# Kernel tuning notes

Hardware: AMD Instinct MI355X
Metric: run time of the kernel (lower is better)

The kernel has to match this reference:

```python
import jax, jax.numpy as jnp
import numpy as np

EPS = 1e-5   # torch nn.LayerNorm default
H = 12       # num_heads


def layernorm(x, w, b):
    m = jnp.mean(x, axis=-1, keepdims=True)
    v = jnp.var(x, axis=-1, keepdims=True)
    return (x - m) * jax.lax.rsqrt(v + EPS) * w + b


def mha(x, qkv_w, proj_w, proj_b):
    # MemEffAttention math (qkv_bias=False, proj_bias=True), block-diagonal mask
    # over equal-length sequences == independent per-row attention.
    B, N, D = x.shape
    hd = D // H
    qkv = jnp.einsum('bnd,ed->bne', x, qkv_w).reshape(B, N, 3, H, hd)
    q, k, v = qkv[:, :, 0], qkv[:, :, 1], qkv[:, :, 2]
    scale = hd ** -0.5
    attn = jnp.einsum('bnhd,bmhd->bhnm', q * scale, k)     # [B,H,N,N]
    attn = jax.nn.softmax(attn, axis=-1)
    o = jnp.einsum('bhnm,bmhd->bnhd', attn, v).reshape(B, N, D)
    return jnp.einsum('bnd,ed->bne', o, proj_w) + proj_b


def block(x, ln1_w, ln1_b, qkv_w, proj_w, proj_b, ln2_w, ln2_b, fc1_w, fc1_b, fc2_w, fc2_b):
    # x = x + attn(norm1(x)); x = x + mlp(norm2(x))  (ls1/ls2 = Identity, eval mode)
    x = x + mha(layernorm(x, ln1_w, ln1_b), qkv_w, proj_w, proj_b)
    h = layernorm(x, ln2_w, ln2_b)
    h = jax.nn.gelu(jnp.einsum('bnd,ed->bne', h, fc1_w) + fc1_b, approximate=False)
    h = jnp.einsum('bne,de->bnd', h, fc2_w) + fc2_b
    return x + h


def setup_inputs() -> dict:
    key = jax.random.key(0)
    ks = jax.random.split(key, 8)
    D, Dff = 768, 3072
    s = lambda k, shape, sc: jax.random.normal(k, shape, jnp.float32) * sc
    return {
        'x1': s(ks[0], (8, 1370, D), 1.0),
        'x2': s(ks[1], (8, 257, D), 1.0),
        'ln1_w': jnp.ones((D,), jnp.float32), 'ln1_b': jnp.zeros((D,), jnp.float32),
        'qkv_w': s(ks[2], (3 * D, D), 0.02),
        'proj_w': s(ks[3], (D, D), 0.02), 'proj_b': jnp.zeros((D,), jnp.float32),
        'ln2_w': jnp.ones((D,), jnp.float32), 'ln2_b': jnp.zeros((D,), jnp.float32),
        'fc1_w': s(ks[4], (Dff, D), 0.02), 'fc1_b': jnp.zeros((Dff,), jnp.float32),
        'fc2_w': s(ks[5], (D, Dff), 0.02), 'fc2_b': jnp.zeros((D,), jnp.float32),
    }


def reference(x1, x2, ln1_w, ln1_b, qkv_w, proj_w, proj_b, ln2_w, ln2_b,
              fc1_w, fc1_b, fc2_w, fc2_b):
    # forward_nested (eval path): block-diagonal attention over nested groups,
    # which factorizes into per-group batched attention; return the
    # concatenated token stream (same values as attn_bias.split output).
    params = (ln1_w, ln1_b, qkv_w, proj_w, proj_b, ln2_w, ln2_b,
              fc1_w, fc1_b, fc2_w, fc2_b)
    o1 = block(x1, *params)
    o2 = block(x2, *params)
    D = x1.shape[-1]
    return jnp.concatenate([o1.reshape(-1, D), o2.reshape(-1, D)], axis=0)
```

## Files before the change

kernel.cpp:

```cpp
#include <hip/hip_runtime.h>
#include <hip/hip_bf16.h>

typedef __attribute__((ext_vector_type(8))) short bf16x8;
typedef __attribute__((ext_vector_type(4))) float f32x4;
typedef __attribute__((ext_vector_type(16))) float f32x16;

#define GL_LDS16(g, l)                                                        \
  __builtin_amdgcn_global_load_lds((const __attribute__((address_space(1))) void*)(g), \
                                   (__attribute__((address_space(3))) void*)(l), 16, 0, 0)

__device__ __forceinline__ ushort f2bf(float f) {
  union { float f; unsigned u; } x; x.f = f;
  unsigned r = x.u + 0x7fffu + ((x.u >> 16) & 1u);
  return (ushort)(r >> 16);
}

__device__ __forceinline__ int xcd_remap(int bid, int nwg) {
  int q = nwg >> 3, r = nwg & 7;
  int xcd = bid & 7, idx = bid >> 3;
  return (xcd < r ? xcd * (q + 1) : r * (q + 1) + (xcd - r) * q) + idx;
}

__global__ void cvt4_kernel(const float* __restrict__ i0, const float* __restrict__ i1,
                            const float* __restrict__ i2, const float* __restrict__ i3,
                            int n0, int n1, int n2, int n3,
                            ushort* __restrict__ out) {
  int c1 = n0 >> 2, c2 = (n0 + n1) >> 2, c3 = (n0 + n1 + n2) >> 2,
      nt = (n0 + n1 + n2 + n3) >> 2;
  int i = blockIdx.x * blockDim.x + threadIdx.x;
  int stride = gridDim.x * blockDim.x;
  for (; i < nt; i += stride) {
    float4 v;
    if (i < c1) v = ((const float4*)i0)[i];
    else if (i < c2) v = ((const float4*)i1)[i - c1];
    else if (i < c3) v = ((const float4*)i2)[i - c2];
    else v = ((const float4*)i3)[i - c3];
    ushort4 o;
    o.x = f2bf(v.x); o.y = f2bf(v.y); o.z = f2bf(v.z); o.w = f2bf(v.w);
    ((ushort4*)out)[i] = o;
  }
}

__global__ __launch_bounds__(256) void ln_kernel(
    const float* __restrict__ x1, const float* __restrict__ x2, int M1, int MT,
    const float* __restrict__ w, const float* __restrict__ b,
    ushort* __restrict__ out) {
  int row = blockIdx.x * 4 + (threadIdx.x >> 6);
  if (row >= MT) return;
  int lane = threadIdx.x & 63;
  const float* xr = (row < M1) ? x1 + (size_t)row * 768
                               : x2 + (size_t)(row - M1) * 768;
  float4 v[3];
  float s = 0.f, sq = 0.f;
#pragma unroll
  for (int i = 0; i < 3; i++) {
    v[i] = *(const float4*)(xr + i * 256 + lane * 4);
    s += v[i].x + v[i].y + v[i].z + v[i].w;
    sq += v[i].x * v[i].x + v[i].y * v[i].y + v[i].z * v[i].z + v[i].w * v[i].w;
  }
#pragma unroll
  for (int m = 1; m < 64; m <<= 1) { s += __shfl_xor(s, m); sq += __shfl_xor(sq, m); }
  float mean = s * (1.f / 768.f);
  float var = sq * (1.f / 768.f) - mean * mean;
  float rstd = rsqrtf(var + 1e-5f);
  ushort* orow = out + (size_t)row * 768;
#pragma unroll
  for (int i = 0; i < 3; i++) {
    int d = i * 256 + lane * 4;
    float4 wv = *(const float4*)(w + d);
    float4 bv = *(const float4*)(b + d);
    ushort4 o;
    o.x = f2bf((v[i].x - mean) * rstd * wv.x + bv.x);
    o.y = f2bf((v[i].y - mean) * rstd * wv.y + bv.y);
    o.z = f2bf((v[i].z - mean) * rstd * wv.z + bv.z);
    o.w = f2bf((v[i].w - mean) * rstd * wv.w + bv.w);
    *(ushort4*)(orow + d) = o;
  }
}

template <int MODE, int K, int NCOL>
__global__ __launch_bounds__(256) void gemm_tile(
    const ushort* __restrict__ A, const ushort* __restrict__ W,
    const float* __restrict__ bias, void* __restrict__ outp,
    int M, int N) {
  __shared__ ushort lA[128 * 64];
  __shared__ ushort lB[128 * 64];
  const int t = threadIdx.x;
  const int lane = t & 63, wave = t >> 6;
  const int l15 = lane & 15, lg = lane >> 4;
  const int waveM = wave >> 1, waveN = wave & 1;
  const int g = xcd_remap(blockIdx.x, gridDim.x);
  const int rowBlk = (g / NCOL) * 128;
  const int colBlk = (g % NCOL) * 128;
  const int srow = t >> 3;
  const int schunk = t & 7;

  f32x4 acc[4][4] = {};

#pragma unroll 1
  for (int k0 = 0; k0 < K; k0 += 64) {
    if (k0) __syncthreads();
#pragma unroll
    for (int i = 0; i < 4; i++) {
      int row = i * 32 + srow;
      int gch = schunk ^ (row & 7);
      GL_LDS16(A + (size_t)(rowBlk + row) * K + k0 + gch * 8,
               &lA[row * 64 + schunk * 8]);
      GL_LDS16(W + (size_t)(colBlk + row) * K + k0 + gch * 8,
               &lB[row * 64 + schunk * 8]);
    }
    __syncthreads();
#pragma unroll
    for (int kk = 0; kk < 2; kk++) {
      bf16x8 af[4], bfr[4];
#pragma unroll
      for (int m = 0; m < 4; m++) {
        int row = waveM * 64 + m * 16 + l15;
        af[m] = *(const bf16x8*)&lA[row * 64 + ((kk * 32 + lg * 8) ^ ((row & 7) << 3))];
      }
#pragma unroll
      for (int c = 0; c < 4; c++) {
        int row = waveN * 64 + c * 16 + l15;
        bfr[c] = *(const bf16x8*)&lB[row * 64 + ((kk * 32 + lg * 8) ^ ((row & 7) << 3))];
      }
      __builtin_amdgcn_s_setprio(1);
#pragma unroll
      for (int m = 0; m < 4; m++)
#pragma unroll
        for (int c = 0; c < 4; c++)
          acc[m][c] = __builtin_amdgcn_mfma_f32_16x16x32_bf16(af[m], bfr[c], acc[m][c], 0, 0, 0);
      __builtin_amdgcn_s_setprio(0);
    }
  }

  const float qsc = (MODE == 0 && colBlk < 768) ? 0.18033688011112042f : 1.f;
#pragma unroll
  for (int m = 0; m < 4; m++) {
    int rowB = rowBlk + waveM * 64 + m * 16 + lg * 4;
#pragma unroll
    for (int c = 0; c < 4; c++) {
      int col = colBlk + waveN * 64 + c * 16 + l15;
      float bv = (MODE == 2) ? bias[col] : 0.f;
#pragma unroll
      for (int j = 0; j < 4; j++) {
        int r = rowB + j;
        if (r < M) {
          float v = acc[m][c][j] + bv;
          size_t idx = (size_t)r * N + col;
          if (MODE == 2) {
            float gl = 0.5f * v * (1.f + erff(v * 0.70710678118f));
            ((ushort*)outp)[idx] = f2bf(gl);
          } else {
            ((ushort*)outp)[idx] = f2bf(v * qsc);
          }
        }
      }
    }
  }
}

template <int K, int NCOL>
__global__ __launch_bounds__(256) void gemm_tile64(
    const ushort* __restrict__ A, const ushort* __restrict__ W,
    const float* __restrict__ bias, const float* __restrict__ res1,
    const float* __restrict__ res2, int resSplit,
    float* __restrict__ outp, int M, int N) {
  __shared__ ushort lA[64 * 64];
  __shared__ ushort lB[128 * 64];
  const int t = threadIdx.x;
  const int lane = t & 63, wave = t >> 6;
  const int l15 = lane & 15, lg = lane >> 4;
  const int waveM = wave >> 1, waveN = wave & 1;
  const int g = xcd_remap(blockIdx.x, gridDim.x);
  const int rowBlk = (g / NCOL) * 64;
  const int colBlk = (g % NCOL) * 128;
  const int srow = t >> 3;
  const int schunk = t & 7;

  f32x4 acc[2][4] = {};

#pragma unroll 1
  for (int k0 = 0; k0 < K; k0 += 64) {
    if (k0) __syncthreads();
#pragma unroll
    for (int i = 0; i < 2; i++) {
      int row = i * 32 + srow;
      int gch = schunk ^ (row & 7);
      GL_LDS16(A + (size_t)(rowBlk + row) * K + k0 + gch * 8,
               &lA[row * 64 + schunk * 8]);
    }
#pragma unroll
    for (int i = 0; i < 4; i++) {
      int row = i * 32 + srow;
      int gch = schunk ^ (row & 7);
      GL_LDS16(W + (size_t)(colBlk + row) * K + k0 + gch * 8,
               &lB[row * 64 + schunk * 8]);
    }
    __syncthreads();
#pragma unroll
    for (int kk = 0; kk < 2; kk++) {
      bf16x8 af[2], bfr[4];
#pragma unroll
      for (int m = 0; m < 2; m++) {
        int row = waveM * 32 + m * 16 + l15;
        af[m] = *(const bf16x8*)&lA[row * 64 + ((kk * 32 + lg * 8) ^ ((row & 7) << 3))];
      }
#pragma unroll
      for (int c = 0; c < 4; c++) {
        int row = waveN * 64 + c * 16 + l15;
        bfr[c] = *(const bf16x8*)&lB[row * 64 + ((kk * 32 + lg * 8) ^ ((row & 7) << 3))];
      }
      __builtin_amdgcn_s_setprio(1);
#pragma unroll
      for (int m = 0; m < 2; m++)
#pragma unroll
        for (int c = 0; c < 4; c++)
          acc[m][c] = __builtin_amdgcn_mfma_f32_16x16x32_bf16(af[m], bfr[c], acc[m][c], 0, 0, 0);
      __builtin_amdgcn_s_setprio(0);
    }
  }

#pragma unroll
  for (int m = 0; m < 2; m++) {
    int rowB = rowBlk + waveM * 32 + m * 16 + lg * 4;
#pragma unroll
    for (int c = 0; c < 4; c++) {
      int col = colBlk + waveN * 64 + c * 16 + l15;
      float bv = bias[col];
#pragma unroll
      for (int j = 0; j < 4; j++) {
        int r = rowB + j;
        if (r < M) {
          size_t idx = (size_t)r * N + col;
          float rv = (r < resSplit) ? res1[idx]
                                    : res2[(size_t)(r - resSplit) * N + col];
          outp[idx] = acc[m][c][j] + bv + rv;
        }
      }
    }
  }
}

__global__ __launch_bounds__(256) void prep_kernel(
    const ushort* __restrict__ qkv, ushort* __restrict__ kt2,
    ushort* __restrict__ vt2, int N1, int N2, int nkv1, int nkv2, int M1) {
  __shared__ ushort lT[64 * 68];
  const int t = threadIdx.x;
  const int bhg = blockIdx.x;
  const int kv = blockIdx.y;
  const int part = bhg >= 96;
  const int bh = part ? bhg - 96 : bhg;
  const int N = part ? N2 : N1;
  const int nkv = part ? nkv2 : nkv1;
  if (kv >= nkv) return;
  const size_t rowbase = part ? (size_t)M1 : 0;
  const int b = bh / 12, h = bh % 12;
  const int k0 = kv * 64;
  const ushort* Kp = qkv + (rowbase + (size_t)b * N) * 2304 + 768 + h * 64;
  const ushort* Vp = Kp + 768;
  size_t tbase = (part ? (size_t)96 * nkv1 : 0) + (size_t)bh * nkv + kv;
  ushort* ktile = kt2 + tbase * 4096;
  ushort* vtile = vt2 + tbase * 4096;
#pragma unroll
  for (int p = 0; p < 2; p++) {
    int s = p * 256 + t;
    int chunk = s >> 6, krow = s & 63;
    ushort4 v0 = {0, 0, 0, 0}, v1 = {0, 0, 0, 0};
    if (k0 + krow < N) {
      const ushort* src = Kp + (size_t)(k0 + krow) * 2304 + chunk * 8;
      v0 = *(const ushort4*)src;
      v1 = *(const ushort4*)(src + 4);
    }
    *(ushort4*)&ktile[s * 8] = v0;
    *(ushort4*)&ktile[s * 8 + 4] = v1;
  }
#pragma unroll
  for (int p = 0; p < 2; p++) {
    int nl = p * 32 + (t >> 3);
    int dc = t & 7;
    ushort4 v0 = {0, 0, 0, 0}, v1 = {0, 0, 0, 0};
    if (k0 + nl < N) {
      const ushort* src = Vp + (size_t)(k0 + nl) * 2304 + dc * 8;
      v0 = *(const ushort4*)src;
      v1 = *(const ushort4*)(src + 4);
    }
    *(ushort4*)&lT[nl * 68 + dc * 8] = v0;
    *(ushort4*)&lT[nl * 68 + dc * 8 + 4] = v1;
  }
  __syncthreads();
#pragma unroll
  for (int p = 0; p < 2; p++) {
    int s = p * 256 + t;
    int kchunk = s >> 6, d = s & 63;
    ushort o[8];
#pragma unroll
    for (int j = 0; j < 8; j++) o[j] = lT[(kchunk * 8 + j) * 68 + d];
    *(ushort4*)&vtile[s * 8] = *(ushort4*)o;
    *(ushort4*)&vtile[s * 8 + 4] = *(ushort4*)(o + 4);
  }
}

#define ATTN_STAGE(buf, kvi)                                                   \
  do {                                                                         \
    _Pragma("unroll") for (int p = 0; p < 2; p++) {                            \
      int s = p * 256 + t;                                                     \
      GL_LDS16(tK + (size_t)(kvi) * 4096 + s * 8, &lK[buf][s * 8]);            \
      GL_LDS16(tV + (size_t)(kvi) * 4096 + s * 8, &lV[buf][s * 8]);            \
    }                                                                          \
  } while (0)

__global__ __launch_bounds__(256) void attn_kernel(
    const ushort* __restrict__ qkv, const ushort* __restrict__ kt2,
    const ushort* __restrict__ vt2, ushort* __restrict__ o_out,
    int N1, int N2, int nkv1, int nkv2, int M1) {
  __shared__ ushort lK[2][4096];
  __shared__ ushort lV[2][4096];
  const int t = threadIdx.x;
  const int lane = t & 63, wave = t >> 6;
  const int l31 = lane & 31, hi = lane >> 5;
  const int bhg = blockIdx.x;
  const int part = bhg >= 96;
  const int bh = part ? bhg - 96 : bhg;
  const int N = part ? N2 : N1;
  const int nkv = part ? nkv2 : nkv1;
  const int qb = blockIdx.y * 128;
  if (qb >= N) return;
  const size_t rowbase = part ? (size_t)M1 : 0;
  const int b = bh / 12, h = bh % 12;
  const ushort* Qp = qkv + (rowbase + (size_t)b * N) * 2304 + h * 64;
  const size_t tboff = (part ? (size_t)96 * nkv1 : 0) + (size_t)bh * nkv;
  const ushort* tK = kt2 + tboff * 4096;
  const ushort* tV = vt2 + tboff * 4096;

  const int qrow = min(qb + wave * 32 + l31, N - 1);
  bf16x8 qf[4];
#pragma unroll
  for (int kc = 0; kc < 4; kc++)
    qf[kc] = *(const bf16x8*)(Qp + (size_t)qrow * 2304 + kc * 16 + hi * 8);

  union { unsigned u[4]; bf16x8 v; } ones;
#pragma unroll
  for (int i = 0; i < 4; i++) ones.u[i] = 0x3F803F80u;

  f32x16 oacc[2] = {};
  f32x16 osum = {};

  ATTN_STAGE(0, 0);
  __syncthreads();
  for (int kv = 0; kv < nkv; kv++) {
    int cur = kv & 1;
    if (kv + 1 < nkv) ATTN_STAGE(cur ^ 1, kv + 1);
    const bool fullTile = (kv * 64 + 64 <= N);
    f32x16 sacc0 = {}, sacc1 = {};
    __builtin_amdgcn_s_setprio(1);
#pragma unroll
    for (int kc = 0; kc < 4; kc++) {
      bf16x8 kf0 = *(const bf16x8*)&lK[cur][(((kc * 2 + hi) << 6) + l31) * 8];
      bf16x8 kf1 = *(const bf16x8*)&lK[cur][(((kc * 2 + hi) << 6) + 32 + l31) * 8];
      sacc0 = __builtin_amdgcn_mfma_f32_32x32x16_bf16(kf0, qf[kc], sacc0, 0, 0, 0);
      sacc1 = __builtin_amdgcn_mfma_f32_32x32x16_bf16(kf1, qf[kc], sacc1, 0, 0, 0);
    }
    __builtin_amdgcn_s_setprio(0);
    float z[32];
#pragma unroll
    for (int r = 0; r < 16; r++) { z[r] = sacc0[r]; z[16 + r] = sacc1[r]; }
    if (!fullTile) {
#pragma unroll
      for (int i = 0; i < 32; i++) {
        int kg = kv * 64 + (i >> 4) * 32 + (i & 3) + (((i & 15) >> 2) << 3) + (hi << 2);
        if (kg >= N) z[i] = -1e30f;
      }
    }
#pragma unroll
    for (int i = 0; i < 32; i++) z[i] = exp2f(z[i]);
#pragma unroll
    for (int kt = 0; kt < 2; kt++) {
      unsigned w0[4], w1[4];
#pragma unroll
      for (int rr = 0; rr < 4; rr++) {
        asm("v_cvt_pk_bf16_f32 %0, %1, %2" : "=v"(w0[rr]) : "v"(z[kt * 16 + 4 * rr]), "v"(z[kt * 16 + 4 * rr + 1]));
        asm("v_cvt_pk_bf16_f32 %0, %1, %2" : "=v"(w1[rr]) : "v"(z[kt * 16 + 4 * rr + 2]), "v"(z[kt * 16 + 4 * rr + 3]));
      }
#pragma unroll
      for (int kc2 = 0; kc2 < 2; kc2++) {
        unsigned ua = w0[2 * kc2], ub = w0[2 * kc2 + 1];
        unsigned uc = w1[2 * kc2], ud = w1[2 * kc2 + 1];
        asm("v_permlane32_swap_b32 %0, %1" : "+&v"(ua), "+v"(ub));
        asm("v_permlane32_swap_b32 %0, %1" : "+&v"(uc), "+v"(ud));
        union { unsigned u[4]; bf16x8 v; } pa;
        pa.u[0] = ua; pa.u[1] = uc; pa.u[2] = ub; pa.u[3] = ud;
        int kcg = kt * 2 + kc2;
        __builtin_amdgcn_s_setprio(1);
#pragma unroll
        for (int dt = 0; dt < 2; dt++) {
          bf16x8 vf = *(const bf16x8*)&lV[cur][(((kcg * 2 + hi) << 6) + dt * 32 + l31) * 8];
          oacc[dt] = __builtin_amdgcn_mfma_f32_32x32x16_bf16(pa.v, vf, oacc[dt], 0, 0, 0);
        }
        osum = __builtin_amdgcn_mfma_f32_32x32x16_bf16(pa.v, ones.v, osum, 0, 0, 0);
        __builtin_amdgcn_s_setprio(0);
      }
    }
    __syncthreads();
  }
#pragma unroll
  for (int r = 0; r < 16; r++) {
    int q = qb + wave * 32 + (r & 3) + ((r >> 2) << 3) + (hi << 2);
    if (q < N) {
      float inv;
      asm("v_rcp_f32 %0, %1" : "=v"(inv) : "v"(osum[r]));
      ushort* orow = o_out + (rowbase + (size_t)b * N + q) * 768 + h * 64;
      orow[l31] = f2bf(oacc[0][r] * inv);
      orow[32 + l31] = f2bf(oacc[1][r] * inv);
    }
  }
}

extern "C" void kernel_launch(void* const* d_in, const int* in_sizes, int n_in,
                              void* d_out, int out_size, void* d_ws, size_t ws_size,
                              hipStream_t stream) {
  const float* x1 = (const float*)d_in[0];
  const float* x2 = (const float*)d_in[1];
  const float* ln1_w = (const float*)d_in[2];
  const float* ln1_b = (const float*)d_in[3];
  const float* qkv_w = (const float*)d_in[4];
  const float* proj_w = (const float*)d_in[5];
  const float* proj_b = (const float*)d_in[6];
  const float* ln2_w = (const float*)d_in[7];
  const float* ln2_b = (const float*)d_in[8];
  const float* fc1_w = (const float*)d_in[9];
  const float* fc1_b = (const float*)d_in[10];
  const float* fc2_w = (const float*)d_in[11];
  const float* fc2_b = (const float*)d_in[12];
  float* out = (float*)d_out;

  const int N1 = 1370, N2 = 257;
  const int M1 = 8 * N1, M2 = 8 * N2;
  const int MT = M1 + M2;
  const int MPAD = 13056;
  const int nkv1 = 22, nkv2 = 5;

  char* ws = (char*)d_ws;
  ushort* wq = (ushort*)ws;   ws += (size_t)2304 * 768 * 2;
  ushort* wp = (ushort*)ws;   ws += (size_t)768 * 768 * 2;
  ushort* w1 = (ushort*)ws;   ws += (size_t)3072 * 768 * 2;
  ushort* w2 = (ushort*)ws;   ws += (size_t)768 * 3072 * 2;
  ushort* bufA = (ushort*)ws;   ws += (size_t)MPAD * 768 * 2;
  ushort* bufQKV = (ushort*)ws; ws += (size_t)MPAD * 2304 * 2;
  ushort* bufFF = (ushort*)ws;  ws += (size_t)MPAD * 3072 * 2;
  const size_t nTiles = (size_t)96 * (nkv1 + nkv2);
  ushort* kt2 = bufFF;
  ushort* vt2 = bufFF + nTiles * 4096;

  cvt4_kernel<<<2048, 256, 0, stream>>>(qkv_w, proj_w, fc1_w, fc2_w,
                                        2304 * 768, 768 * 768, 3072 * 768, 768 * 3072, wq);

  ln_kernel<<<(MT + 3) / 4, 256, 0, stream>>>(x1, x2, M1, MT, ln1_w, ln1_b, bufA);
  gemm_tile<0, 768, 18><<<(MPAD / 128) * 18, 256, 0, stream>>>(
      bufA, wq, nullptr, bufQKV, MT, 2304);
  prep_kernel<<<dim3(192, nkv1), 256, 0, stream>>>(bufQKV, kt2, vt2, N1, N2, nkv1, nkv2, M1);
  attn_kernel<<<dim3(192, 11), 256, 0, stream>>>(
      bufQKV, kt2, vt2, bufA, N1, N2, nkv1, nkv2, M1);
  gemm_tile64<768, 6><<<(MPAD / 64) * 6, 256, 0, stream>>>(
      bufA, wp, proj_b, x1, x2, M1, out, MT, 768);
  ln_kernel<<<(MT + 3) / 4, 256, 0, stream>>>(out, out, MT, MT, ln2_w, ln2_b, bufA);
  gemm_tile<2, 768, 24><<<(MPAD / 128) * 24, 256, 0, stream>>>(
      bufA, w1, fc1_b, bufFF, MT, 3072);
  gemm_tile64<3072, 6><<<(MPAD / 64) * 6, 256, 0, stream>>>(
      bufFF, w2, fc2_b, out, nullptr, MT, out, MT, 768);
}
```

Baseline: 459.0 us.

## Double-buffer LDS in GEMM kernels with vmcnt-based prefetch pipelining

Both GEMM kernels now keep two LDS buffers and issue global-to-LDS loads two k-steps ahead. Partial vmcnt waits plus explicit barriers let the next tile's loads overlap the current tile's MFMA work. The goal is to hide global memory latency that the old per-step load-then-sync loop exposed. In exchange, LDS use doubles, which may cut occupancy. The hand-counted vmcnt values also rely on the exact number of loads issued per stage.

```diff
diff --git a/kernel.cpp b/kernel.cpp
--- a/kernel.cpp
+++ b/kernel.cpp
@@ -8,6 +8,9 @@
 #define GL_LDS16(g, l)                                                        \
   __builtin_amdgcn_global_load_lds((const __attribute__((address_space(1))) void*)(g), \
                                    (__attribute__((address_space(3))) void*)(l), 16, 0, 0)
+
+#define VM_BAR(N) asm volatile("s_waitcnt vmcnt(" #N ")\ns_barrier" ::: "memory")
+#define LGKM_BAR() asm volatile("s_waitcnt lgkmcnt(0)\ns_barrier" ::: "memory")
 
 __device__ __forceinline__ ushort f2bf(float f) {
   union { float f; unsigned u; } x; x.f = f;
@@ -78,13 +81,46 @@
   }
 }
 
+#define GT_STAGE(buf, tstep)                                                   \
+  do {                                                                         \
+    int k0s = (tstep) << 6;                                                    \
+    _Pragma("unroll") for (int i = 0; i < 4; i++) {                            \
+      int row = i * 32 + srow;                                                 \
+      int gch = schunk ^ (row & 7);                                            \
+      GL_LDS16(A + (size_t)(rowBlk + row) * K + k0s + gch * 8,                 \
+               &lA[buf][row * 64 + schunk * 8]);                               \
+      GL_LDS16(W + (size_t)(colBlk + row) * K + k0s + gch * 8,                 \
+               &lB[buf][row * 64 + schunk * 8]);                               \
+    }                                                                          \
+  } while (0)
+
+#define GT_COMPUTE(cbuf)                                                       \
+  do {                                                                         \
+    _Pragma("unroll") for (int kk = 0; kk < 2; kk++) {                         \
+      bf16x8 af[4], bfr[4];                                                    \
+      _Pragma("unroll") for (int m = 0; m < 4; m++) {                          \
+        int row = waveM * 64 + m * 16 + l15;                                   \
+        af[m] = *(const bf16x8*)&lA[cbuf][row * 64 + ((kk * 32 + lg * 8) ^ ((row & 7) << 3))]; \
+      }                                                                        \
+      _Pragma("unroll") for (int cc = 0; cc < 4; cc++) {                       \
+        int row = waveN * 64 + cc * 16 + l15;                                  \
+        bfr[cc] = *(const bf16x8*)&lB[cbuf][row * 64 + ((kk * 32 + lg * 8) ^ ((row & 7) << 3))]; \
+      }                                                                        \
+      __builtin_amdgcn_s_setprio(1);                                           \
+      _Pragma("unroll") for (int m = 0; m < 4; m++)                            \
+        _Pragma("unroll") for (int cc = 0; cc < 4; cc++)                       \
+          acc[m][cc] = __builtin_amdgcn_mfma_f32_16x16x32_bf16(af[m], bfr[cc], acc[m][cc], 0, 0, 0); \
+      __builtin_amdgcn_s_setprio(0);                                           \
+    }                                                                          \
+  } while (0)
+
 template <int MODE, int K, int NCOL>
 __global__ __launch_bounds__(256) void gemm_tile(
     const ushort* __restrict__ A, const ushort* __restrict__ W,
     const float* __restrict__ bias, void* __restrict__ outp,
     int M, int N) {
-  __shared__ ushort lA[128 * 64];
-  __shared__ ushort lB[128 * 64];
+  __shared__ ushort lA[2][128 * 64];
+  __shared__ ushort lB[2][128 * 64];
   const int t = threadIdx.x;
   const int lane = t & 63, wave = t >> 6;
   const int l15 = lane & 15, lg = lane >> 4;
@@ -96,42 +132,20 @@
   const int schunk = t & 7;
 
   f32x4 acc[4][4] = {};
-
+  constexpr int nt = K >> 6;
+
+  GT_STAGE(0, 0);
+  GT_STAGE(1, 1);
 #pragma unroll 1
-  for (int k0 = 0; k0 < K; k0 += 64) {
-    if (k0) __syncthreads();
-#pragma unroll
-    for (int i = 0; i < 4; i++) {
-      int row = i * 32 + srow;
-      int gch = schunk ^ (row & 7);
-      GL_LDS16(A + (size_t)(rowBlk + row) * K + k0 + gch * 8,
-               &lA[row * 64 + schunk * 8]);
-      GL_LDS16(W + (size_t)(colBlk + row) * K + k0 + gch * 8,
-               &lB[row * 64 + schunk * 8]);
-    }
-    __syncthreads();
-#pragma unroll
-    for (int kk = 0; kk < 2; kk++) {
-      bf16x8 af[4], bfr[4];
-#pragma unroll
-      for (int m = 0; m < 4; m++) {
-        int row = waveM * 64 + m * 16 + l15;
-        af[m] = *(const bf16x8*)&lA[row * 64 + ((kk * 32 + lg * 8) ^ ((row & 7) << 3))];
-      }
-#pragma unroll
-      for (int c = 0; c < 4; c++) {
-        int row = waveN * 64 + c * 16 + l15;
-        bfr[c] = *(const bf16x8*)&lB[row * 64 + ((kk * 32 + lg * 8) ^ ((row & 7) << 3))];
-      }
-      __builtin_amdgcn_s_setprio(1);
-#pragma unroll
-      for (int m = 0; m < 4; m++)
-#pragma unroll
-        for (int c = 0; c < 4; c++)
-          acc[m][c] = __builtin_amdgcn_mfma_f32_16x16x32_bf16(af[m], bfr[c], acc[m][c], 0, 0, 0);
-      __builtin_amdgcn_s_setprio(0);
-    }
-  }
+  for (int tt = 0; tt < nt - 1; ++tt) {
+    const int cur = tt & 1;
+    VM_BAR(8);
+    GT_COMPUTE(cur);
+    LGKM_BAR();
+    if (tt + 2 < nt) GT_STAGE(cur, tt + 2);
+  }
+  VM_BAR(0);
+  GT_COMPUTE((nt - 1) & 1);
 
   const float qsc = (MODE == 0 && colBlk < 768) ? 0.18033688011112042f : 1.f;
 #pragma unroll
@@ -159,14 +173,51 @@
   }
 }
 
+#define G64_STAGE(buf, tstep)                                                  \
+  do {                                                                         \
+    int k0s = (tstep) << 6;                                                    \
+    _Pragma("unroll") for (int i = 0; i < 2; i++) {                            \
+      int row = i * 32 + srow;                                                 \
+      int gch = schunk ^ (row & 7);                                            \
+      GL_LDS16(A + (size_t)(rowBlk + row) * K + k0s + gch * 8,                 \
+               &lA[buf][row * 64 + schunk * 8]);                               \
+    }                                                                          \
+    _Pragma("unroll") for (int i = 0; i < 4; i++) {                            \
+      int row = i * 32 + srow;                                                 \
+      int gch = schunk ^ (row & 7);                                            \
+      GL_LDS16(W + (size_t)(colBlk + row) * K + k0s + gch * 8,                 \
+               &lB[buf][row * 64 + schunk * 8]);                               \
+    }                                                                          \
+  } while (0)
+
+#define G64_COMPUTE(cbuf)                                                      \
+  do {                                                                         \
+    _Pragma("unroll") for (int kk = 0; kk < 2; kk++) {                         \
+      bf16x8 af[2], bfr[4];                                                    \
+      _Pragma("unroll") for (int m = 0; m < 2; m++) {                          \
+        int row = waveM * 32 + m * 16 + l15;                                   \
+        af[m] = *(const bf16x8*)&lA[cbuf][row * 64 + ((kk * 32 + lg * 8) ^ ((row & 7) << 3))]; \
+      }                                                                        \
+      _Pragma("unroll") for (int cc = 0; cc < 4; cc++) {                       \
+        int row = waveN * 64 + cc * 16 + l15;                                  \
+        bfr[cc] = *(const bf16x8*)&lB[cbuf][row * 64 + ((kk * 32 + lg * 8) ^ ((row & 7) << 3))]; \
+      }                                                                        \
+      __builtin_amdgcn_s_setprio(1);                                           \
+      _Pragma("unroll") for (int m = 0; m < 2; m++)                            \
+        _Pragma("unroll") for (int cc = 0; cc < 4; cc++)                       \
+          acc[m][cc] = __builtin_amdgcn_mfma_f32_16x16x32_bf16(af[m], bfr[cc], acc[m][cc], 0, 0, 0); \
+      __builtin_amdgcn_s_setprio(0);                                           \
+    }                                                                          \
+  } while (0)
+
 template <int K, int NCOL>
 __global__ __launch_bounds__(256) void gemm_tile64(
     const ushort* __restrict__ A, const ushort* __restrict__ W,
     const float* __restrict__ bias, const float* __restrict__ res1,
     const float* __restrict__ res2, int resSplit,
     float* __restrict__ outp, int M, int N) {
-  __shared__ ushort lA[64 * 64];
-  __shared__ ushort lB[128 * 64];
+  __shared__ ushort lA[2][64 * 64];
+  __shared__ ushort lB[2][128 * 64];
   const int t = threadIdx.x;
   const int lane = t & 63, wave = t >> 6;
   const int l15 = lane & 15, lg = lane >> 4;
@@ -178,47 +229,20 @@
   const int schunk = t & 7;
 
   f32x4 acc[2][4] = {};
-
+  constexpr int nt = K >> 6;
+
+  G64_STAGE(0, 0);
+  G64_STAGE(1, 1);
 #pragma unroll 1
-  for (int k0 = 0; k0 < K; k0 += 64) {
-    if (k0) __syncthreads();
-#pragma unroll
-    for (int i = 0; i < 2; i++) {
-      int row = i * 32 + srow;
-      int gch = schunk ^ (row & 7);
-      GL_LDS16(A + (size_t)(rowBlk + row) * K + k0 + gch * 8,
-               &lA[row * 64 + schunk * 8]);
-    }
-#pragma unroll
-    for (int i = 0; i < 4; i++) {
-      int row = i * 32 + srow;
-      int gch = schunk ^ (row & 7);
-      GL_LDS16(W + (size_t)(colBlk + row) * K + k0 + gch * 8,
-               &lB[row * 64 + schunk * 8]);
-    }
-    __syncthreads();
-#pragma unroll
-    for (int kk = 0; kk < 2; kk++) {
-      bf16x8 af[2], bfr[4];
-#pragma unroll
-      for (int m = 0; m < 2; m++) {
-        int row = waveM * 32 + m * 16 + l15;
-        af[m] = *(const bf16x8*)&lA[row * 64 + ((kk * 32 + lg * 8) ^ ((row & 7) << 3))];
-      }
-#pragma unroll
-      for (int c = 0; c < 4; c++) {
-        int row = waveN * 64 + c * 16 + l15;
-        bfr[c] = *(const bf16x8*)&lB[row * 64 + ((kk * 32 + lg * 8) ^ ((row & 7) << 3))];
-      }
-      __builtin_amdgcn_s_setprio(1);
-#pragma unroll
-      for (int m = 0; m < 2; m++)
-#pragma unroll
-        for (int c = 0; c < 4; c++)
-          acc[m][c] = __builtin_amdgcn_mfma_f32_16x16x32_bf16(af[m], bfr[c], acc[m][c], 0, 0, 0);
-      __builtin_amdgcn_s_setprio(0);
-    }
-  }
+  for (int tt = 0; tt < nt - 1; ++tt) {
+    const int cur = tt & 1;
+    VM_BAR(6);
+    G64_COMPUTE(cur);
+    LGKM_BAR();
+    if (tt + 2 < nt) G64_STAGE(cur, tt + 2);
+  }
+  VM_BAR(0);
+  G64_COMPUTE((nt - 1) & 1);
 
 #pragma unroll
   for (int m = 0; m < 2; m++) {
```

Result: slower. 524.3 us (+14.2%).
